# Performance work log

Hardware: AMD Instinct MI355X
Metric: run time of the kernel (lower is better)

## Reference

```python
import jax, jax.numpy as jnp
import numpy as np

N_NODES = 1_000_000
N_EDGES = 16_000_000


def setup_inputs() -> dict:
    key = jax.random.key(0)
    ks = jax.random.split(key, 12)
    feat = jax.random.normal(ks[0], (N_NODES, 1), dtype=jnp.float32)
    # symmetric GCN norm D^{-1/2}; positive values in (0, 1]
    norm = jax.random.uniform(ks[1], (N_NODES, 1), dtype=jnp.float32, minval=0.05, maxval=1.0)
    src = jax.random.randint(ks[2], (N_EDGES,), 0, N_NODES, dtype=jnp.int32)
    dst = jax.random.randint(ks[3], (N_EDGES,), 0, N_NODES, dtype=jnp.int32)
    dims = [(1, 3), (3, 3), (3, 3), (3, 3), (3, 3), (3, 1)]
    params = {}
    for i, (fi, fo) in enumerate(dims):
        w = jax.random.normal(ks[4 + i], (fi, fo), dtype=jnp.float32) * (1.0 / np.sqrt(fi))
        params[f"W{i+1}"] = w
        params[f"b{i+1}"] = jnp.zeros((fo,), dtype=jnp.float32)
    return dict(feat=feat, norm=norm, src=src, dst=dst, **params)


def _gcn_layer(h, norm, W, b, src, dst, n_nodes):
    # DGL-style GraphConv with symmetric norm:
    #   h = h * norm; agg_i = sum_{(j->i) in E} h_j; h = agg * norm; h = h @ W + b; relu
    h = h * norm                                   # [N, F]
    msgs = jnp.take(h, src, axis=0)                # [E, F] irregular gather
    agg = jax.ops.segment_sum(msgs, dst, num_segments=n_nodes)  # [N, F] scatter-add
    agg = agg * norm
    return jax.nn.relu(agg @ W + b)


def reference(feat, norm, W1, b1, W2, b2, W3, b3, W4, b4, W5, b5, W6, b6, src, dst):
    n = feat.shape[0]
    h = feat
    for W, b in ((W1, b1), (W2, b2), (W3, b3), (W4, b4), (W5, b5), (W6, b6)):
        h = _gcn_layer(h, norm, W, b, src, dst, n)
    return h  # [N, 1]
```

## Files before the change

kernel.cpp:

```cpp
#include <hip/hip_runtime.h>


#define BT 256
#define NBLK 256
#define BSHIFT 12
#define BSIZE 4096
#define LMASK 4095
#define NBKT 256
#define M (NBLK * NBKT)
#define BTL 1024

__global__ void k_init(const float* __restrict__ feat, const float* __restrict__ norm,
                       float* __restrict__ s0, int N) {
  int i = blockIdx.x * BT + threadIdx.x;
  if (i < N) s0[i] = feat[i] * norm[i];
}

__global__ void k_phist(const int* __restrict__ dst, int* __restrict__ histB,
                        int E, int chunk) {
  __shared__ int h[NBKT];
  if (threadIdx.x < NBKT) h[threadIdx.x] = 0;
  __syncthreads();
  int b = blockIdx.x;
  int beg = b * chunk, end = min(beg + chunk, E);
  int i = beg + (int)threadIdx.x * 4;
  for (; i + 3 < end; i += BT * 4) {
    int4 v = *(const int4*)(dst + i);
    atomicAdd(&h[v.x >> BSHIFT], 1);
    atomicAdd(&h[v.y >> BSHIFT], 1);
    atomicAdd(&h[v.z >> BSHIFT], 1);
    atomicAdd(&h[v.w >> BSHIFT], 1);
  }
  for (; i < end; ++i) atomicAdd(&h[dst[i] >> BSHIFT], 1);
  __syncthreads();
  if (threadIdx.x < NBKT) histB[b * NBKT + threadIdx.x] = h[threadIdx.x];
}

__global__ void k_transp(const int* __restrict__ in, int* __restrict__ out, int R, int C) {
  __shared__ int tile[64][65];
  int c0 = blockIdx.x * 64, r0 = blockIdx.y * 64;
  int tx = threadIdx.x & 63, ty = threadIdx.x >> 6;
  for (int j = 0; j < 16; ++j) {
    int r = ty + j * 4;
    tile[r][tx] = in[(r0 + r) * C + c0 + tx];
  }
  __syncthreads();
  for (int j = 0; j < 16; ++j) {
    int r = ty + j * 4;
    out[(c0 + r) * R + r0 + tx] = tile[tx][r];
  }
}

__global__ void k_blockSum(const int* __restrict__ data, int* __restrict__ partial, int Mlen) {
  __shared__ int tmp[BT];
  int i = blockIdx.x * BT + threadIdx.x;
  tmp[threadIdx.x] = (i < Mlen) ? data[i] : 0;
  __syncthreads();
  for (int off = BT / 2; off > 0; off >>= 1) {
    if (threadIdx.x < off) tmp[threadIdx.x] += tmp[threadIdx.x + off];
    __syncthreads();
  }
  if (threadIdx.x == 0) partial[blockIdx.x] = tmp[0];
}

__global__ void k_scanPartials(int* __restrict__ partial, int nb) {
  __shared__ int tmp[BT];
  __shared__ int carry;
  int t = threadIdx.x;
  if (t == 0) carry = 0;
  __syncthreads();
  for (int base = 0; base < nb; base += BT) {
    int i = base + t;
    int v = (i < nb) ? partial[i] : 0;
    tmp[t] = v;
    __syncthreads();
    for (int off = 1; off < BT; off <<= 1) {
      int x = 0;
      if (t >= off) x = tmp[t - off];
      __syncthreads();
      tmp[t] += x;
      __syncthreads();
    }
    if (i < nb) partial[i] = tmp[t] - v + carry;
    __syncthreads();
    if (t == BT - 1) carry += tmp[BT - 1];
    __syncthreads();
  }
}

__global__ void k_scanFinal(int* __restrict__ data, const int* __restrict__ partial, int Mlen) {
  __shared__ int tmp[BT];
  int t = threadIdx.x;
  int i = blockIdx.x * BT + t;
  int v = (i < Mlen) ? data[i] : 0;
  tmp[t] = v;
  __syncthreads();
  for (int off = 1; off < BT; off <<= 1) {
    int x = 0;
    if (t >= off) x = tmp[t - off];
    __syncthreads();
    tmp[t] += x;
    __syncthreads();
  }
  if (i < Mlen) data[i] = tmp[t] - v + partial[blockIdx.x];
}

__global__ void k_pscatter(const int* __restrict__ src, const int* __restrict__ dst,
                           const int* __restrict__ scanT, unsigned int* __restrict__ packed,
                           int E, int chunk) {
  __shared__ int cur[NBKT];
  int b = blockIdx.x;
  if (threadIdx.x < NBKT) cur[threadIdx.x] = scanT[b * NBKT + threadIdx.x];
  __syncthreads();
  int beg = b * chunk, end = min(beg + chunk, E);
  int i = beg + (int)threadIdx.x * 4;
  for (; i + 3 < end; i += BT * 4) {
    int4 u = *(const int4*)(src + i);
    int4 v = *(const int4*)(dst + i);
    int p;
    p = atomicAdd(&cur[v.x >> BSHIFT], 1);
    packed[p] = ((unsigned)u.x << BSHIFT) | (unsigned)(v.x & LMASK);
    p = atomicAdd(&cur[v.y >> BSHIFT], 1);
    packed[p] = ((unsigned)u.y << BSHIFT) | (unsigned)(v.y & LMASK);
    p = atomicAdd(&cur[v.z >> BSHIFT], 1);
    packed[p] = ((unsigned)u.z << BSHIFT) | (unsigned)(v.z & LMASK);
    p = atomicAdd(&cur[v.w >> BSHIFT], 1);
    packed[p] = ((unsigned)u.w << BSHIFT) | (unsigned)(v.w & LMASK);
  }
  for (; i < end; ++i) {
    int p = atomicAdd(&cur[dst[i] >> BSHIFT], 1);
    packed[p] = ((unsigned)src[i] << BSHIFT) | (unsigned)(dst[i] & LMASK);
  }
}


#define ACC3(p)                                             \
  {                                                         \
    unsigned pp = (p);                                      \
    float4 m = ((const float4*)sPrev)[pp >> BSHIFT];        \
    int loc = pp & LMASK;                                   \
    atomicAdd(&a0[loc], m.x);                               \
    atomicAdd(&a1[loc], m.y);                               \
    atomicAdd(&a2[loc], m.z);                               \
  }

#define ACC1(p)                                             \
  {                                                         \
    unsigned pp = (p);                                      \
    atomicAdd(&a[pp & LMASK], sIn[pp >> BSHIFT]);           \
  }

__global__ __launch_bounds__(BTL) void k_layer1(
    const int* __restrict__ scanT, const unsigned int* __restrict__ packed,
    const float* __restrict__ sIn, const float* __restrict__ norm,
    const float* __restrict__ W1, const float* __restrict__ b1,
    float* __restrict__ sNext, int N) {
  __shared__ float a[BSIZE];
  int k = blockIdx.x;
  for (int i = threadIdx.x; i < BSIZE; i += BTL) a[i] = 0.0f;
  int beg = scanT[k], end = scanT[k + 1];
  __syncthreads();
  int abeg = min(end, (beg + 3) & ~3);
  int t = beg + (int)threadIdx.x;
  if (t < abeg) ACC1(packed[t]);
  int i = abeg + (int)threadIdx.x * 4;
  for (; i + 3 < end; i += BTL * 4) {
    uint4 p4 = *(const uint4*)(packed + i);
    ACC1(p4.x) ACC1(p4.y) ACC1(p4.z) ACC1(p4.w)
  }
  for (; i < end; ++i) ACC1(packed[i]);
  __syncthreads();
  int node0 = k << BSHIFT;
  for (int tt = threadIdx.x; tt < BSIZE; tt += BTL) {
    int node = node0 + tt;
    if (node >= N) break;
    float n = norm[node];
    float pre = a[tt] * n;
    float h0 = fmaxf(0.0f, pre * W1[0] + b1[0]);
    float h1 = fmaxf(0.0f, pre * W1[1] + b1[1]);
    float h2 = fmaxf(0.0f, pre * W1[2] + b1[2]);
    ((float4*)sNext)[node] = make_float4(h0 * n, h1 * n, h2 * n, 0.0f);
  }
}

__global__ __launch_bounds__(BTL) void k_layer3(
    const int* __restrict__ scanT, const unsigned int* __restrict__ packed,
    const float* __restrict__ sPrev, const float* __restrict__ norm,
    const float* __restrict__ W, const float* __restrict__ bias,
    float* __restrict__ sNext, int N) {
  __shared__ float a0[BSIZE], a1[BSIZE], a2[BSIZE];
  int k = blockIdx.x;
  for (int i = threadIdx.x; i < BSIZE; i += BTL) { a0[i] = 0.0f; a1[i] = 0.0f; a2[i] = 0.0f; }
  int beg = scanT[k], end = scanT[k + 1];
  __syncthreads();
  int abeg = min(end, (beg + 3) & ~3);
  int t = beg + (int)threadIdx.x;
  if (t < abeg) ACC3(packed[t]);
  int i = abeg + (int)threadIdx.x * 4;
  for (; i + 3 < end; i += BTL * 4) {
    uint4 p4 = *(const uint4*)(packed + i);
    ACC3(p4.x) ACC3(p4.y) ACC3(p4.z) ACC3(p4.w)
  }
  for (; i < end; ++i) ACC3(packed[i]);
  __syncthreads();
  int node0 = k << BSHIFT;
  for (int tt = threadIdx.x; tt < BSIZE; tt += BTL) {
    int node = node0 + tt;
    if (node >= N) break;
    float n = norm[node];
    float x0 = a0[tt] * n, x1 = a1[tt] * n, x2 = a2[tt] * n;
    float h0 = fmaxf(0.0f, x0 * W[0] + x1 * W[3] + x2 * W[6] + bias[0]);
    float h1 = fmaxf(0.0f, x0 * W[1] + x1 * W[4] + x2 * W[7] + bias[1]);
    float h2 = fmaxf(0.0f, x0 * W[2] + x1 * W[5] + x2 * W[8] + bias[2]);
    ((float4*)sNext)[node] = make_float4(h0 * n, h1 * n, h2 * n, 0.0f);
  }
}

__global__ __launch_bounds__(BTL) void k_layer5(
    const int* __restrict__ scanT, const unsigned int* __restrict__ packed,
    const float* __restrict__ sPrev, const float* __restrict__ norm,
    const float* __restrict__ W5, const float* __restrict__ b5,
    const float* __restrict__ W6, float* __restrict__ sB, int N) {
  __shared__ float a0[BSIZE], a1[BSIZE], a2[BSIZE];
  int k = blockIdx.x;
  for (int i = threadIdx.x; i < BSIZE; i += BTL) { a0[i] = 0.0f; a1[i] = 0.0f; a2[i] = 0.0f; }
  int beg = scanT[k], end = scanT[k + 1];
  __syncthreads();
  int abeg = min(end, (beg + 3) & ~3);
  int t = beg + (int)threadIdx.x;
  if (t < abeg) ACC3(packed[t]);
  int i = abeg + (int)threadIdx.x * 4;
  for (; i + 3 < end; i += BTL * 4) {
    uint4 p4 = *(const uint4*)(packed + i);
    ACC3(p4.x) ACC3(p4.y) ACC3(p4.z) ACC3(p4.w)
  }
  for (; i < end; ++i) ACC3(packed[i]);
  __syncthreads();
  int node0 = k << BSHIFT;
  for (int tt = threadIdx.x; tt < BSIZE; tt += BTL) {
    int node = node0 + tt;
    if (node >= N) break;
    float n = norm[node];
    float x0 = a0[tt] * n, x1 = a1[tt] * n, x2 = a2[tt] * n;
    float h0 = fmaxf(0.0f, x0 * W5[0] + x1 * W5[3] + x2 * W5[6] + b5[0]);
    float h1 = fmaxf(0.0f, x0 * W5[1] + x1 * W5[4] + x2 * W5[7] + b5[1]);
    float h2 = fmaxf(0.0f, x0 * W5[2] + x1 * W5[5] + x2 * W5[8] + b5[2]);
    sB[node] = (h0 * W6[0] + h1 * W6[1] + h2 * W6[2]) * n;
  }
}

__global__ __launch_bounds__(BTL) void k_layer6(
    const int* __restrict__ scanT, const unsigned int* __restrict__ packed,
    const float* __restrict__ sIn, const float* __restrict__ norm,
    const float* __restrict__ b6, float* __restrict__ out, int N) {
  __shared__ float a[BSIZE];
  int k = blockIdx.x;
  for (int i = threadIdx.x; i < BSIZE; i += BTL) a[i] = 0.0f;
  int beg = scanT[k], end = scanT[k + 1];
  __syncthreads();
  int abeg = min(end, (beg + 3) & ~3);
  int t = beg + (int)threadIdx.x;
  if (t < abeg) ACC1(packed[t]);
  int i = abeg + (int)threadIdx.x * 4;
  for (; i + 3 < end; i += BTL * 4) {
    uint4 p4 = *(const uint4*)(packed + i);
    ACC1(p4.x) ACC1(p4.y) ACC1(p4.z) ACC1(p4.w)
  }
  for (; i < end; ++i) ACC1(packed[i]);
  __syncthreads();
  int node0 = k << BSHIFT;
  for (int tt = threadIdx.x; tt < BSIZE; tt += BTL) {
    int node = node0 + tt;
    if (node >= N) break;
    out[node] = fmaxf(0.0f, a[tt] * norm[node] + b6[0]);
  }
}

extern "C" void kernel_launch(void* const* d_in, const int* in_sizes, int n_in,
                              void* d_out, int out_size, void* d_ws, size_t ws_size,
                              hipStream_t stream) {
  const float* feat = (const float*)d_in[0];
  const float* norm = (const float*)d_in[1];
  const int* src = (const int*)d_in[2];
  const int* dst = (const int*)d_in[3];
  const float* W1 = (const float*)d_in[4];
  const float* b1 = (const float*)d_in[5];
  const float* W2 = (const float*)d_in[6];
  const float* b2 = (const float*)d_in[7];
  const float* W3 = (const float*)d_in[8];
  const float* b3 = (const float*)d_in[9];
  const float* W4 = (const float*)d_in[10];
  const float* b4 = (const float*)d_in[11];
  const float* W5 = (const float*)d_in[12];
  const float* b5 = (const float*)d_in[13];
  const float* W6 = (const float*)d_in[14];
  const float* b6 = (const float*)d_in[15];
  float* out = (float*)d_out;

  const int N = in_sizes[0];
  const int E = in_sizes[2];
  const int nbNode = (N + BT - 1) / BT;
  const int nBkt = (N + BSIZE - 1) >> BSHIFT;
  const int chunk = (((E + NBLK - 1) / NBLK) + 3) & ~3;

  unsigned int* packed = (unsigned int*)d_ws;
  int* histB = (int*)(packed + (size_t)E);
  int* histT = histB + (size_t)M;
  int* scanT = histT + (size_t)M;
  int* partial = scanT + (size_t)M;
  float* s0B = (float*)(partial + M / BT);
  float* sA = s0B + (size_t)N;
  float* sA2 = sA + (size_t)4 * N;

  k_init<<<nbNode, BT, 0, stream>>>(feat, norm, s0B, N);
  k_phist<<<NBLK, BT, 0, stream>>>(dst, histB, E, chunk);
  {
    dim3 g1(NBKT / 64, NBLK / 64);
    k_transp<<<g1, BT, 0, stream>>>(histB, histT, NBLK, NBKT);
  }
  k_blockSum<<<M / BT, BT, 0, stream>>>(histT, partial, M);
  k_scanPartials<<<1, BT, 0, stream>>>(partial, M / BT);
  k_scanFinal<<<M / BT, BT, 0, stream>>>(histT, partial, M);
  {
    dim3 g2(NBLK / 64, NBKT / 64);
    k_transp<<<g2, BT, 0, stream>>>(histT, scanT, NBKT, NBLK);
  }
  k_pscatter<<<NBLK, BT, 0, stream>>>(src, dst, scanT, packed, E, chunk);

  k_layer1<<<nBkt, BTL, 0, stream>>>(scanT, packed, s0B, norm, W1, b1, sA, N);
  k_layer3<<<nBkt, BTL, 0, stream>>>(scanT, packed, sA, norm, W2, b2, sA2, N);
  k_layer3<<<nBkt, BTL, 0, stream>>>(scanT, packed, sA2, norm, W3, b3, sA, N);
  k_layer3<<<nBkt, BTL, 0, stream>>>(scanT, packed, sA, norm, W4, b4, sA2, N);
  k_layer5<<<nBkt, BTL, 0, stream>>>(scanT, packed, sA2, norm, W5, b5, W6, s0B, N);
  k_layer6<<<nBkt, BTL, 0, stream>>>(scanT, packed, s0B, norm, b6, out, N);
}
```

Measured before the change: 1.556 ms.

## Sub-sort edges within each destination bucket by source range for gather locality

The partitioning key becomes a combination of the destination bucket and the top two bits of the source index, giving four sub-bins per destination bucket. Within each bucket's edge range, edges are grouped by source quarter, so the gathers in each layer kernel touch a smaller window of the feature array at any given time, which should improve L2 hit rates. The cost is a histogram and scan four times larger and an extra src read in the histogram pass.

```diff
diff --git a/kernel.cpp b/kernel.cpp
--- a/kernel.cpp
+++ b/kernel.cpp
@@ -6,9 +6,14 @@
 #define BSHIFT 12
 #define BSIZE 4096
 #define LMASK 4095
-#define NBKT 256
-#define M (NBLK * NBKT)
+#define SSH 18
+#define NBINS 1024
+#define M (NBLK * NBINS)
 #define BTL 1024
+
+__device__ __forceinline__ int edge_key(int s, int d) {
+  return ((d >> BSHIFT) << 2) | (s >> SSH);
+}
 
 __global__ void k_init(const float* __restrict__ feat, const float* __restrict__ norm,
                        float* __restrict__ s0, int N) {
@@ -16,24 +21,25 @@
   if (i < N) s0[i] = feat[i] * norm[i];
 }
 
-__global__ void k_phist(const int* __restrict__ dst, int* __restrict__ histB,
-                        int E, int chunk) {
-  __shared__ int h[NBKT];
-  if (threadIdx.x < NBKT) h[threadIdx.x] = 0;
+__global__ void k_phist(const int* __restrict__ src, const int* __restrict__ dst,
+                        int* __restrict__ histB, int E, int chunk) {
+  __shared__ int h[NBINS];
+  for (int i = threadIdx.x; i < NBINS; i += BT) h[i] = 0;
   __syncthreads();
   int b = blockIdx.x;
   int beg = b * chunk, end = min(beg + chunk, E);
   int i = beg + (int)threadIdx.x * 4;
   for (; i + 3 < end; i += BT * 4) {
+    int4 u = *(const int4*)(src + i);
     int4 v = *(const int4*)(dst + i);
-    atomicAdd(&h[v.x >> BSHIFT], 1);
-    atomicAdd(&h[v.y >> BSHIFT], 1);
-    atomicAdd(&h[v.z >> BSHIFT], 1);
-    atomicAdd(&h[v.w >> BSHIFT], 1);
-  }
-  for (; i < end; ++i) atomicAdd(&h[dst[i] >> BSHIFT], 1);
-  __syncthreads();
-  if (threadIdx.x < NBKT) histB[b * NBKT + threadIdx.x] = h[threadIdx.x];
+    atomicAdd(&h[edge_key(u.x, v.x)], 1);
+    atomicAdd(&h[edge_key(u.y, v.y)], 1);
+    atomicAdd(&h[edge_key(u.z, v.z)], 1);
+    atomicAdd(&h[edge_key(u.w, v.w)], 1);
+  }
+  for (; i < end; ++i) atomicAdd(&h[edge_key(src[i], dst[i])], 1);
+  __syncthreads();
+  for (int k = threadIdx.x; k < NBINS; k += BT) histB[b * NBINS + k] = h[k];
 }
 
 __global__ void k_transp(const int* __restrict__ in, int* __restrict__ out, int R, int C) {
@@ -108,9 +114,9 @@
 __global__ void k_pscatter(const int* __restrict__ src, const int* __restrict__ dst,
                            const int* __restrict__ scanT, unsigned int* __restrict__ packed,
                            int E, int chunk) {
-  __shared__ int cur[NBKT];
+  __shared__ int cur[NBINS];
   int b = blockIdx.x;
-  if (threadIdx.x < NBKT) cur[threadIdx.x] = scanT[b * NBKT + threadIdx.x];
+  for (int k = threadIdx.x; k < NBINS; k += BT) cur[k] = scanT[b * NBINS + k];
   __syncthreads();
   int beg = b * chunk, end = min(beg + chunk, E);
   int i = beg + (int)threadIdx.x * 4;
@@ -118,17 +124,17 @@
     int4 u = *(const int4*)(src + i);
     int4 v = *(const int4*)(dst + i);
     int p;
-    p = atomicAdd(&cur[v.x >> BSHIFT], 1);
+    p = atomicAdd(&cur[edge_key(u.x, v.x)], 1);
     packed[p] = ((unsigned)u.x << BSHIFT) | (unsigned)(v.x & LMASK);
-    p = atomicAdd(&cur[v.y >> BSHIFT], 1);
+    p = atomicAdd(&cur[edge_key(u.y, v.y)], 1);
     packed[p] = ((unsigned)u.y << BSHIFT) | (unsigned)(v.y & LMASK);
-    p = atomicAdd(&cur[v.z >> BSHIFT], 1);
+    p = atomicAdd(&cur[edge_key(u.z, v.z)], 1);
     packed[p] = ((unsigned)u.z << BSHIFT) | (unsigned)(v.z & LMASK);
-    p = atomicAdd(&cur[v.w >> BSHIFT], 1);
+    p = atomicAdd(&cur[edge_key(u.w, v.w)], 1);
     packed[p] = ((unsigned)u.w << BSHIFT) | (unsigned)(v.w & LMASK);
   }
   for (; i < end; ++i) {
-    int p = atomicAdd(&cur[dst[i] >> BSHIFT], 1);
+    int p = atomicAdd(&cur[edge_key(src[i], dst[i])], 1);
     packed[p] = ((unsigned)src[i] << BSHIFT) | (unsigned)(dst[i] & LMASK);
   }
 }
@@ -158,7 +164,7 @@
   __shared__ float a[BSIZE];
   int k = blockIdx.x;
   for (int i = threadIdx.x; i < BSIZE; i += BTL) a[i] = 0.0f;
-  int beg = scanT[k], end = scanT[k + 1];
+  int beg = scanT[k << 2], end = scanT[(k << 2) + 4];
   __syncthreads();
   int abeg = min(end, (beg + 3) & ~3);
   int t = beg + (int)threadIdx.x;
@@ -191,7 +197,7 @@
   __shared__ float a0[BSIZE], a1[BSIZE], a2[BSIZE];
   int k = blockIdx.x;
   for (int i = threadIdx.x; i < BSIZE; i += BTL) { a0[i] = 0.0f; a1[i] = 0.0f; a2[i] = 0.0f; }
-  int beg = scanT[k], end = scanT[k + 1];
+  int beg = scanT[k << 2], end = scanT[(k << 2) + 4];
   __syncthreads();
   int abeg = min(end, (beg + 3) & ~3);
   int t = beg + (int)threadIdx.x;
@@ -224,7 +230,7 @@
   __shared__ float a0[BSIZE], a1[BSIZE], a2[BSIZE];
   int k = blockIdx.x;
   for (int i = threadIdx.x; i < BSIZE; i += BTL) { a0[i] = 0.0f; a1[i] = 0.0f; a2[i] = 0.0f; }
-  int beg = scanT[k], end = scanT[k + 1];
+  int beg = scanT[k << 2], end = scanT[(k << 2) + 4];
   __syncthreads();
   int abeg = min(end, (beg + 3) & ~3);
   int t = beg + (int)threadIdx.x;
@@ -256,7 +262,7 @@
   __shared__ float a[BSIZE];
   int k = blockIdx.x;
   for (int i = threadIdx.x; i < BSIZE; i += BTL) a[i] = 0.0f;
-  int beg = scanT[k], end = scanT[k + 1];
+  int beg = scanT[k << 2], end = scanT[(k << 2) + 4];
   __syncthreads();
   int abeg = min(end, (beg + 3) & ~3);
   int t = beg + (int)threadIdx.x;
@@ -313,17 +319,17 @@
   float* sA2 = sA + (size_t)4 * N;
 
   k_init<<<nbNode, BT, 0, stream>>>(feat, norm, s0B, N);
-  k_phist<<<NBLK, BT, 0, stream>>>(dst, histB, E, chunk);
+  k_phist<<<NBLK, BT, 0, stream>>>(src, dst, histB, E, chunk);
   {
-    dim3 g1(NBKT / 64, NBLK / 64);
-    k_transp<<<g1, BT, 0, stream>>>(histB, histT, NBLK, NBKT);
+    dim3 g1(NBINS / 64, NBLK / 64);
+    k_transp<<<g1, BT, 0, stream>>>(histB, histT, NBLK, NBINS);
   }
   k_blockSum<<<M / BT, BT, 0, stream>>>(histT, partial, M);
   k_scanPartials<<<1, BT, 0, stream>>>(partial, M / BT);
   k_scanFinal<<<M / BT, BT, 0, stream>>>(histT, partial, M);
   {
-    dim3 g2(NBLK / 64, NBKT / 64);
-    k_transp<<<g2, BT, 0, stream>>>(histT, scanT, NBKT, NBLK);
+    dim3 g2(NBLK / 64, NBINS / 64);
+    k_transp<<<g2, BT, 0, stream>>>(histT, scanT, NBINS, NBLK);
   }
   k_pscatter<<<NBLK, BT, 0, stream>>>(src, dst, scanT, packed, E, chunk);
 
```

After: 1.547 ms. About the same (-0.6%).

## Sort edges within each dst bucket by source range and unroll gathers by eight

Applied to the files above, without the earlier changes.

Adds a per-bucket counting sort (k_sortB) that reorders each bucket's packed edges by the high bits of the source index, so the gathers in the six layer kernels touch sPrev in a more localized order with better cache reuse. Each layer kernel now loads eight packed entries and issues all eight gathers before the shared-memory atomics, to expose more memory-level parallelism. The sort is an extra pass over packed that relies on a large per-thread register array (CAP=72). Buckets larger than CAP*BTL are left unsorted, and the sort may not pay for itself across only six layers.

```diff
diff --git a/kernel.cpp b/kernel.cpp
--- a/kernel.cpp
+++ b/kernel.cpp
@@ -9,6 +9,8 @@
 #define NBKT 256
 #define M (NBLK * NBKT)
 #define BTL 1024
+#define NSB 16384
+#define CAP 72
 
 __global__ void k_init(const float* __restrict__ feat, const float* __restrict__ norm,
                        float* __restrict__ s0, int N) {
@@ -133,6 +135,59 @@
   }
 }
 
+__global__ __launch_bounds__(BTL) void k_sortB(const int* __restrict__ scanT,
+                                               unsigned int* __restrict__ packed) {
+  __shared__ int cnt[NSB];
+  __shared__ int tsum[BTL];
+  int k = blockIdx.x;
+  int beg = scanT[k], end = scanT[k + 1];
+  if (end - beg > CAP * BTL) return;
+  int t = threadIdx.x;
+  for (int i = t; i < NSB; i += BTL) cnt[i] = 0;
+  __syncthreads();
+  unsigned e[CAP];
+#pragma unroll
+  for (int j = 0; j < CAP; ++j) {
+    int i = beg + t + j * BTL;
+    if (i < end) {
+      unsigned p = packed[i];
+      e[j] = p;
+      atomicAdd(&cnt[p >> 18], 1);
+    }
+  }
+  __syncthreads();
+  int base16 = t * 16;
+  int s = 0;
+#pragma unroll
+  for (int j = 0; j < 16; ++j) s += cnt[base16 + j];
+  tsum[t] = s;
+  __syncthreads();
+  for (int off = 1; off < BTL; off <<= 1) {
+    int x = 0;
+    if (t >= off) x = tsum[t - off];
+    __syncthreads();
+    tsum[t] += x;
+    __syncthreads();
+  }
+  int run = tsum[t] - s;
+#pragma unroll
+  for (int j = 0; j < 16; ++j) {
+    int c = cnt[base16 + j];
+    cnt[base16 + j] = run;
+    run += c;
+  }
+  __syncthreads();
+#pragma unroll
+  for (int j = 0; j < CAP; ++j) {
+    int i = beg + t + j * BTL;
+    if (i < end) {
+      unsigned p = e[j];
+      int pos = atomicAdd(&cnt[p >> 18], 1);
+      packed[beg + pos] = p;
+    }
+  }
+}
+
 
 #define ACC3(p)                                             \
   {                                                         \
@@ -160,13 +215,31 @@
   for (int i = threadIdx.x; i < BSIZE; i += BTL) a[i] = 0.0f;
   int beg = scanT[k], end = scanT[k + 1];
   __syncthreads();
-  int abeg = min(end, (beg + 3) & ~3);
-  int t = beg + (int)threadIdx.x;
-  if (t < abeg) ACC1(packed[t]);
-  int i = abeg + (int)threadIdx.x * 4;
-  for (; i + 3 < end; i += BTL * 4) {
-    uint4 p4 = *(const uint4*)(packed + i);
-    ACC1(p4.x) ACC1(p4.y) ACC1(p4.z) ACC1(p4.w)
+  int abeg = min(end, (beg + 7) & ~7);
+  {
+    int t = beg + (int)threadIdx.x;
+    if (t < abeg) ACC1(packed[t]);
+  }
+  int i = abeg + (int)threadIdx.x * 8;
+  for (; i + 7 < end; i += BTL * 8) {
+    uint4 pa = *(const uint4*)(packed + i);
+    uint4 pb = *(const uint4*)(packed + i + 4);
+    float m0 = sIn[pa.x >> BSHIFT];
+    float m1 = sIn[pa.y >> BSHIFT];
+    float m2 = sIn[pa.z >> BSHIFT];
+    float m3 = sIn[pa.w >> BSHIFT];
+    float m4 = sIn[pb.x >> BSHIFT];
+    float m5 = sIn[pb.y >> BSHIFT];
+    float m6 = sIn[pb.z >> BSHIFT];
+    float m7 = sIn[pb.w >> BSHIFT];
+    atomicAdd(&a[pa.x & LMASK], m0);
+    atomicAdd(&a[pa.y & LMASK], m1);
+    atomicAdd(&a[pa.z & LMASK], m2);
+    atomicAdd(&a[pa.w & LMASK], m3);
+    atomicAdd(&a[pb.x & LMASK], m4);
+    atomicAdd(&a[pb.y & LMASK], m5);
+    atomicAdd(&a[pb.z & LMASK], m6);
+    atomicAdd(&a[pb.w & LMASK], m7);
   }
   for (; i < end; ++i) ACC1(packed[i]);
   __syncthreads();
@@ -193,13 +266,31 @@
   for (int i = threadIdx.x; i < BSIZE; i += BTL) { a0[i] = 0.0f; a1[i] = 0.0f; a2[i] = 0.0f; }
   int beg = scanT[k], end = scanT[k + 1];
   __syncthreads();
-  int abeg = min(end, (beg + 3) & ~3);
-  int t = beg + (int)threadIdx.x;
-  if (t < abeg) ACC3(packed[t]);
-  int i = abeg + (int)threadIdx.x * 4;
-  for (; i + 3 < end; i += BTL * 4) {
-    uint4 p4 = *(const uint4*)(packed + i);
-    ACC3(p4.x) ACC3(p4.y) ACC3(p4.z) ACC3(p4.w)
+  int abeg = min(end, (beg + 7) & ~7);
+  {
+    int t = beg + (int)threadIdx.x;
+    if (t < abeg) ACC3(packed[t]);
+  }
+  int i = abeg + (int)threadIdx.x * 8;
+  for (; i + 7 < end; i += BTL * 8) {
+    uint4 pa = *(const uint4*)(packed + i);
+    uint4 pb = *(const uint4*)(packed + i + 4);
+    float4 m0 = ((const float4*)sPrev)[pa.x >> BSHIFT];
+    float4 m1 = ((const float4*)sPrev)[pa.y >> BSHIFT];
+    float4 m2 = ((const float4*)sPrev)[pa.z >> BSHIFT];
+    float4 m3 = ((const float4*)sPrev)[pa.w >> BSHIFT];
+    float4 m4 = ((const float4*)sPrev)[pb.x >> BSHIFT];
+    float4 m5 = ((const float4*)sPrev)[pb.y >> BSHIFT];
+    float4 m6 = ((const float4*)sPrev)[pb.z >> BSHIFT];
+    float4 m7 = ((const float4*)sPrev)[pb.w >> BSHIFT];
+    atomicAdd(&a0[pa.x & LMASK], m0.x); atomicAdd(&a1[pa.x & LMASK], m0.y); atomicAdd(&a2[pa.x & LMASK], m0.z);
+    atomicAdd(&a0[pa.y & LMASK], m1.x); atomicAdd(&a1[pa.y & LMASK], m1.y); atomicAdd(&a2[pa.y & LMASK], m1.z);
+    atomicAdd(&a0[pa.z & LMASK], m2.x); atomicAdd(&a1[pa.z & LMASK], m2.y); atomicAdd(&a2[pa.z & LMASK], m2.z);
+    atomicAdd(&a0[pa.w & LMASK], m3.x); atomicAdd(&a1[pa.w & LMASK], m3.y); atomicAdd(&a2[pa.w & LMASK], m3.z);
+    atomicAdd(&a0[pb.x & LMASK], m4.x); atomicAdd(&a1[pb.x & LMASK], m4.y); atomicAdd(&a2[pb.x & LMASK], m4.z);
+    atomicAdd(&a0[pb.y & LMASK], m5.x); atomicAdd(&a1[pb.y & LMASK], m5.y); atomicAdd(&a2[pb.y & LMASK], m5.z);
+    atomicAdd(&a0[pb.z & LMASK], m6.x); atomicAdd(&a1[pb.z & LMASK], m6.y); atomicAdd(&a2[pb.z & LMASK], m6.z);
+    atomicAdd(&a0[pb.w & LMASK], m7.x); atomicAdd(&a1[pb.w & LMASK], m7.y); atomicAdd(&a2[pb.w & LMASK], m7.z);
   }
   for (; i < end; ++i) ACC3(packed[i]);
   __syncthreads();
@@ -226,13 +317,31 @@
   for (int i = threadIdx.x; i < BSIZE; i += BTL) { a0[i] = 0.0f; a1[i] = 0.0f; a2[i] = 0.0f; }
   int beg = scanT[k], end = scanT[k + 1];
   __syncthreads();
-  int abeg = min(end, (beg + 3) & ~3);
-  int t = beg + (int)threadIdx.x;
-  if (t < abeg) ACC3(packed[t]);
-  int i = abeg + (int)threadIdx.x * 4;
-  for (; i + 3 < end; i += BTL * 4) {
-    uint4 p4 = *(const uint4*)(packed + i);
-    ACC3(p4.x) ACC3(p4.y) ACC3(p4.z) ACC3(p4.w)
+  int abeg = min(end, (beg + 7) & ~7);
+  {
+    int t = beg + (int)threadIdx.x;
+    if (t < abeg) ACC3(packed[t]);
+  }
+  int i = abeg + (int)threadIdx.x * 8;
+  for (; i + 7 < end; i += BTL * 8) {
+    uint4 pa = *(const uint4*)(packed + i);
+    uint4 pb = *(const uint4*)(packed + i + 4);
+    float4 m0 = ((const float4*)sPrev)[pa.x >> BSHIFT];
+    float4 m1 = ((const float4*)sPrev)[pa.y >> BSHIFT];
+    float4 m2 = ((const float4*)sPrev)[pa.z >> BSHIFT];
+    float4 m3 = ((const float4*)sPrev)[pa.w >> BSHIFT];
+    float4 m4 = ((const float4*)sPrev)[pb.x >> BSHIFT];
+    float4 m5 = ((const float4*)sPrev)[pb.y >> BSHIFT];
+    float4 m6 = ((const float4*)sPrev)[pb.z >> BSHIFT];
+    float4 m7 = ((const float4*)sPrev)[pb.w >> BSHIFT];
+    atomicAdd(&a0[pa.x & LMASK], m0.x); atomicAdd(&a1[pa.x & LMASK], m0.y); atomicAdd(&a2[pa.x & LMASK], m0.z);
+    atomicAdd(&a0[pa.y & LMASK], m1.x); atomicAdd(&a1[pa.y & LMASK], m1.y); atomicAdd(&a2[pa.y & LMASK], m1.z);
+    atomicAdd(&a0[pa.z & LMASK], m2.x); atomicAdd(&a1[pa.z & LMASK], m2.y); atomicAdd(&a2[pa.z & LMASK], m2.z);
+    atomicAdd(&a0[pa.w & LMASK], m3.x); atomicAdd(&a1[pa.w & LMASK], m3.y); atomicAdd(&a2[pa.w & LMASK], m3.z);
+    atomicAdd(&a0[pb.x & LMASK], m4.x); atomicAdd(&a1[pb.x & LMASK], m4.y); atomicAdd(&a2[pb.x & LMASK], m4.z);
+    atomicAdd(&a0[pb.y & LMASK], m5.x); atomicAdd(&a1[pb.y & LMASK], m5.y); atomicAdd(&a2[pb.y & LMASK], m5.z);
+    atomicAdd(&a0[pb.z & LMASK], m6.x); atomicAdd(&a1[pb.z & LMASK], m6.y); atomicAdd(&a2[pb.z & LMASK], m6.z);
+    atomicAdd(&a0[pb.w & LMASK], m7.x); atomicAdd(&a1[pb.w & LMASK], m7.y); atomicAdd(&a2[pb.w & LMASK], m7.z);
   }
   for (; i < end; ++i) ACC3(packed[i]);
   __syncthreads();
@@ -258,13 +367,31 @@
   for (int i = threadIdx.x; i < BSIZE; i += BTL) a[i] = 0.0f;
   int beg = scanT[k], end = scanT[k + 1];
   __syncthreads();
-  int abeg = min(end, (beg + 3) & ~3);
-  int t = beg + (int)threadIdx.x;
-  if (t < abeg) ACC1(packed[t]);
-  int i = abeg + (int)threadIdx.x * 4;
-  for (; i + 3 < end; i += BTL * 4) {
-    uint4 p4 = *(const uint4*)(packed + i);
-    ACC1(p4.x) ACC1(p4.y) ACC1(p4.z) ACC1(p4.w)
+  int abeg = min(end, (beg + 7) & ~7);
+  {
+    int t = beg + (int)threadIdx.x;
+    if (t < abeg) ACC1(packed[t]);
+  }
+  int i = abeg + (int)threadIdx.x * 8;
+  for (; i + 7 < end; i += BTL * 8) {
+    uint4 pa = *(const uint4*)(packed + i);
+    uint4 pb = *(const uint4*)(packed + i + 4);
+    float m0 = sIn[pa.x >> BSHIFT];
+    float m1 = sIn[pa.y >> BSHIFT];
+    float m2 = sIn[pa.z >> BSHIFT];
+    float m3 = sIn[pa.w >> BSHIFT];
+    float m4 = sIn[pb.x >> BSHIFT];
+    float m5 = sIn[pb.y >> BSHIFT];
+    float m6 = sIn[pb.z >> BSHIFT];
+    float m7 = sIn[pb.w >> BSHIFT];
+    atomicAdd(&a[pa.x & LMASK], m0);
+    atomicAdd(&a[pa.y & LMASK], m1);
+    atomicAdd(&a[pa.z & LMASK], m2);
+    atomicAdd(&a[pa.w & LMASK], m3);
+    atomicAdd(&a[pb.x & LMASK], m4);
+    atomicAdd(&a[pb.y & LMASK], m5);
+    atomicAdd(&a[pb.z & LMASK], m6);
+    atomicAdd(&a[pb.w & LMASK], m7);
   }
   for (; i < end; ++i) ACC1(packed[i]);
   __syncthreads();
@@ -326,6 +453,7 @@
     k_transp<<<g2, BT, 0, stream>>>(histT, scanT, NBKT, NBLK);
   }
   k_pscatter<<<NBLK, BT, 0, stream>>>(src, dst, scanT, packed, E, chunk);
+  k_sortB<<<nBkt, BTL, 0, stream>>>(scanT, packed);
 
   k_layer1<<<nBkt, BTL, 0, stream>>>(scanT, packed, s0B, norm, W1, b1, sA, N);
   k_layer3<<<nBkt, BTL, 0, stream>>>(scanT, packed, sA, norm, W2, b2, sA2, N);
```

Result: slower. 1.760 ms (+13.1%).
